# Kernel tuning notes

Hardware: AMD Instinct MI355X
Metric: run time of the kernel (lower is better)

## Reference

```python
import jax, jax.numpy as jnp
import numpy as np

N = 50000        # nodes
E = 800000       # edges (avg degree 16)
F_IN = 11        # raw node features
HID = 128        # hidden_dim
HEADS = 4
C = HID // HEADS # per-head channels = 32
L = 4            # num_layers
NEG_SLOPE = 0.2  # PyG GATv2 default


def setup_inputs() -> dict:
    key = jax.random.key(0)
    ks = jax.random.split(key, 10)
    s = 0.1
    node_features = jax.random.normal(ks[0], (N, F_IN), jnp.float32)
    edge_index = jax.random.randint(ks[1], (2, E), 0, N, dtype=jnp.int32)
    W_emb = jax.random.normal(ks[2], (HID, F_IN), jnp.float32) * s
    b_emb = jnp.zeros((HID,), jnp.float32)
    Wl = jax.random.normal(ks[3], (L, HID, HID), jnp.float32) * s
    bl = jnp.zeros((L, HID), jnp.float32)
    Wr = jax.random.normal(ks[4], (L, HID, HID), jnp.float32) * s
    br = jnp.zeros((L, HID), jnp.float32)
    att = jax.random.normal(ks[5], (L, HEADS, C), jnp.float32) * s
    bias = jnp.zeros((L, HID), jnp.float32)
    return {
        "node_features": node_features, "edge_index": edge_index, "num_nodes": N,
        "W_emb": W_emb, "b_emb": b_emb, "Wl": Wl, "bl": bl,
        "Wr": Wr, "br": br, "att": att, "bias": bias,
    }


def _gatv2_layer(x, src, dst, Wl, bl, Wr, br, att, bias):
    """PyG GATv2Conv (concat=True, share_weights=False), dropout off."""
    n = x.shape[0]
    xl = (x @ Wl.T + bl).reshape(n, HEADS, C)  # source transform
    xr = (x @ Wr.T + br).reshape(n, HEADS, C)  # target transform
    e = jax.nn.leaky_relu(xl[src] + xr[dst], NEG_SLOPE)       # [E,H,C]
    logits = jnp.einsum('ehc,hc->eh', e, att)                 # [E,H]
    # segment softmax over incoming edges per destination node
    m = jax.ops.segment_max(logits, dst, num_segments=n)      # [N,H]
    m = jnp.where(jnp.isfinite(m), m, jnp.zeros_like(m))      # empty segments
    p = jnp.exp(logits - m[dst])                              # [E,H]
    denom = jax.ops.segment_sum(p, dst, num_segments=n)       # [N,H]
    alpha = p / denom[dst]
    out = jax.ops.segment_sum(alpha[:, :, None] * xl[src], dst, num_segments=n)
    return out.reshape(n, HID) + bias


def reference(node_features, edge_index, num_nodes, W_emb, b_emb, Wl, bl, Wr, br, att, bias):
    src, dst = edge_index[0], edge_index[1]
    x = jax.nn.relu(node_features @ W_emb.T + b_emb)
    for i in range(L):  # BatchNorms exist in the torch module but are never applied
        x_res = x
        x = _gatv2_layer(x, src, dst, Wl[i], bl[i], Wr[i], br[i], att[i], bias[i])
        x = jax.nn.relu(x)
        if i > 0:
            x = x + x_res
    graph_mean = jnp.mean(x, axis=0)
    graph_max = jnp.max(x, axis=0)
    graph_embedding = jnp.concatenate([graph_mean, graph_max], axis=-1)  # [2*HID]
    return graph_embedding, x
```

## Files before the change

### kernel.cpp

```cpp
#include <hip/hip_runtime.h>
#include <math.h>

#define HID 128
#define HEADS 4
#define NEG_SLOPE 0.2f
#define R1B 1024
#define BCAP 8192
#define PB 6144
#define ACHUNK 4096

typedef float f32x4 __attribute__((ext_vector_type(4)));
typedef _Float16 f16x8 __attribute__((ext_vector_type(8)));
typedef _Float16 f16x4 __attribute__((ext_vector_type(4)));
typedef _Float16 f16x2 __attribute__((ext_vector_type(2)));

#if defined(__has_builtin)
#if __has_builtin(__builtin_amdgcn_fdot2)
#define HAVE_FDOT2 1
#endif
#endif


__global__ __launch_bounds__(256) void k_zero_int(int* p, int n) {
    int i = blockIdx.x * blockDim.x + threadIdx.x;
    if (i < n) p[i] = 0;
}

__global__ __launch_bounds__(256) void k_binA(const int* __restrict__ src, const int* __restrict__ dst,
                                              int E, int* __restrict__ gcnt, int* __restrict__ arena) {
    __shared__ int lh[256];
    __shared__ int lbase[256];
    __shared__ unsigned short lrank[ACHUNK];
    const int tid = threadIdx.x;
    lh[tid] = 0;
    __syncthreads();
    const int e0 = blockIdx.x * ACHUNK;
    #pragma unroll
    for (int i = 0; i < ACHUNK / 256; i++) {
        int e = e0 + i * 256 + tid;
        if (e < E) {
            int b = dst[e] >> 8;
            lrank[i * 256 + tid] = (unsigned short)atomicAdd(&lh[b], 1);
        }
    }
    __syncthreads();
    if (lh[tid] > 0) lbase[tid] = atomicAdd(&gcnt[tid], lh[tid]);
    __syncthreads();
    #pragma unroll
    for (int i = 0; i < ACHUNK / 256; i++) {
        int e = e0 + i * 256 + tid;
        if (e < E) {
            int d = dst[e];
            int b = d >> 8;
            arena[b * BCAP + lbase[b] + lrank[i * 256 + tid]] = (src[e] << 8) | (d & 255);
        }
    }
}

__global__ __launch_bounds__(256) void k_scan_bk(const int* __restrict__ gcnt, int nbk,
                                                 int* __restrict__ bstart, int* __restrict__ rowptr,
                                                 int N, int E) {
    __shared__ int buf[256];
    int tid = threadIdx.x;
    int v = (tid < nbk) ? gcnt[tid] : 0;
    buf[tid] = v;
    __syncthreads();
    for (int off = 1; off < 256; off <<= 1) {
        int t = (tid >= off) ? buf[tid - off] : 0;
        __syncthreads();
        buf[tid] += t;
        __syncthreads();
    }
    bstart[tid] = buf[tid] - v;
    if (tid == 0) rowptr[N] = E;
}

__global__ __launch_bounds__(256) void k_binB(const int* __restrict__ arena, const int* __restrict__ gcnt,
                                              const int* __restrict__ bstart, int N,
                                              int* __restrict__ rowptr, int* __restrict__ csr_off) {
    __shared__ int ncnt[256];
    __shared__ int sbuf[256];
    __shared__ int nstart[256];
    __shared__ int stage[PB];
    __shared__ unsigned short rk[BCAP];
    const int b = blockIdx.x, tid = threadIdx.x;
    const int cnt = gcnt[b];
    const int seg = bstart[b];
    ncnt[tid] = 0;
    __syncthreads();
    for (int k = tid; k < cnt; k += 256) {
        int v = arena[b * BCAP + k];
        rk[k] = (unsigned short)atomicAdd(&ncnt[v & 255], 1);
    }
    __syncthreads();
    int c = ncnt[tid];
    sbuf[tid] = c;
    __syncthreads();
    for (int off = 1; off < 256; off <<= 1) {
        int t = (tid >= off) ? sbuf[tid - off] : 0;
        __syncthreads();
        sbuf[tid] += t;
        __syncthreads();
    }
    int myStart = sbuf[tid] - c;
    nstart[tid] = myStart;
    int n = b * 256 + tid;
    if (n < N) rowptr[n] = seg + myStart;
    __syncthreads();
    for (int k = tid; k < cnt; k += 256) {
        int v = arena[b * BCAP + k];
        int pos = nstart[v & 255] + rk[k];
        int val = v & 0xFFFFFF00;
        if (pos < PB) stage[pos] = val;
        else          csr_off[seg + pos] = val;
    }
    __syncthreads();
    int lim = min(cnt, PB);
    for (int k = tid; k < lim; k += 256) csr_off[seg + k] = stage[k];
}


__device__ inline f16x2 absh2(f16x2 v) {
    unsigned u = __builtin_bit_cast(unsigned, v) & 0x7FFF7FFFu;
    return __builtin_bit_cast(f16x2, u);
}

template <int CTRL>
__device__ inline float qp_xor_add(float x) {
    int y = __builtin_amdgcn_update_dpp(0, __builtin_bit_cast(int, x),
                                        CTRL, 0xF, 0xF, true);
    return x + __builtin_bit_cast(float, y);
}

__device__ inline float edge_logit(f16x2 c0, f16x2 c1, f16x2 c2, f16x2 c3,
                                   f16x2 xr0, f16x2 xr1, f16x2 xr2, f16x2 xr3,
                                   f16x2 a0, f16x2 a1, f16x2 a2, f16x2 a3) {
    const f16x2 k06 = (f16x2){(_Float16)0.6f, (_Float16)0.6f};
    const f16x2 k04 = (f16x2){(_Float16)0.4f, (_Float16)0.4f};
    f16x2 u0 = c0 + xr0, u1 = c1 + xr1, u2 = c2 + xr2, u3 = c3 + xr3;
    f16x2 l0 = u0 * k06 + absh2(u0) * k04;
    f16x2 l1 = u1 * k06 + absh2(u1) * k04;
    f16x2 l2 = u2 * k06 + absh2(u2) * k04;
    f16x2 l3 = u3 * k06 + absh2(u3) * k04;
#ifdef HAVE_FDOT2
    float p = __builtin_amdgcn_fdot2(l0, a0, 0.f, false);
    p = __builtin_amdgcn_fdot2(l1, a1, p, false);
    p = __builtin_amdgcn_fdot2(l2, a2, p, false);
    p = __builtin_amdgcn_fdot2(l3, a3, p, false);
#else
    float p = (float)l0[0] * (float)a0[0] + (float)l0[1] * (float)a0[1]
            + (float)l1[0] * (float)a1[0] + (float)l1[1] * (float)a1[1]
            + (float)l2[0] * (float)a2[0] + (float)l2[1] * (float)a2[1]
            + (float)l3[0] * (float)a3[0] + (float)l3[1] * (float)a3[1];
#endif
    return p;
}

__global__ __launch_bounds__(256) void k_tof16(const float* __restrict__ a, const float* __restrict__ b,
                                               _Float16* __restrict__ oa, _Float16* __restrict__ ob, int n) {
    const float* x = blockIdx.y ? b : a;
    _Float16*    o = blockIdx.y ? ob : oa;
    int base = (blockIdx.x * 256 + threadIdx.x) * 4;
    if (base >= n) return;
    float4 v = *(const float4*)(x + base);
    f16x4 h = {(_Float16)v.x, (_Float16)v.y, (_Float16)v.z, (_Float16)v.w};
    *(f16x4*)(o + base) = h;
}


__global__ __launch_bounds__(512) void k_linear_mfma(
        const _Float16* __restrict__ xh,
        const _Float16* __restrict__ WfL, const _Float16* __restrict__ WfR,
        const float* __restrict__ bl, const float* __restrict__ br,
        _Float16* __restrict__ xlh, _Float16* __restrict__ xrh, int N) {
    __shared__ _Float16 lds[16384];
    const int t   = threadIdx.x;
    const int mat = blockIdx.y;
    const _Float16* W = mat ? WfR : WfL;

    for (int g = t; g < 2048; g += 512) {
        int r = g >> 4, cc = g & 15;
        int dsto = r * 128 + ((cc ^ (r & 7)) << 3);
        *(float4*)&lds[dsto] = *(const float4*)(W + g * 8);
    }
    __syncthreads();

    const int wave = t >> 6;
    const int lane = t & 63;
    const int l16  = lane & 15;
    const int quad = lane >> 4;
    const int n0   = blockIdx.x * 256 + wave * 32;

    int arow0 = n0 + l16;
    int arow1 = n0 + 16 + l16;
    if (arow0 >= N) arow0 = N - 1;
    if (arow1 >= N) arow1 = N - 1;

    f32x4 acc[2][8];
    #pragma unroll
    for (int u = 0; u < 2; u++)
        #pragma unroll
        for (int s = 0; s < 8; s++) acc[u][s] = (f32x4){0.f, 0.f, 0.f, 0.f};

    #pragma unroll
    for (int k0 = 0; k0 < HID; k0 += 32) {
        f16x8 a0 = *(const f16x8*)(xh + arow0 * HID + k0 + quad * 8);
        f16x8 a1 = *(const f16x8*)(xh + arow1 * HID + k0 + quad * 8);
        const int cc = (k0 >> 3) + quad;
        #pragma unroll
        for (int s = 0; s < 8; s++) {
            const int row = s * 16 + l16;
            const int off = row * 128 + ((cc ^ (l16 & 7)) << 3);
            f16x8 b = *(const f16x8*)&lds[off];
            acc[0][s] = __builtin_amdgcn_mfma_f32_16x16x32_f16(a0, b, acc[0][s], 0, 0, 0);
            acc[1][s] = __builtin_amdgcn_mfma_f32_16x16x32_f16(a1, b, acc[1][s], 0, 0, 0);
        }
    }

    const float* bias = mat ? br : bl;
    _Float16* dst = mat ? xrh : xlh;
    #pragma unroll
    for (int s = 0; s < 8; s++) {
        int col = s * 16 + l16;
        float bv = bias[col];
        #pragma unroll
        for (int u = 0; u < 2; u++) {
            #pragma unroll
            for (int r = 0; r < 4; r++) {
                int node = n0 + u * 16 + quad * 4 + r;
                if (node < N) dst[(size_t)node * HID + col] = (_Float16)(acc[u][s][r] + bv);
            }
        }
    }
}


__global__ __launch_bounds__(256, 8) void k_attn(const _Float16* __restrict__ xlh, const _Float16* __restrict__ xrh,
                                              const int* __restrict__ rowptr, const int* __restrict__ csr_off,
                                              const float* __restrict__ att, const float* __restrict__ bias,
                                              const _Float16* __restrict__ xres, _Float16* __restrict__ outx,
                                              float* __restrict__ out,
                                              int add_res, int want_half, int N) {
    const int wave = threadIdx.x >> 6;
    const int lane = threadIdx.x & 63;
    const int strm = lane >> 4;
    const int l16  = lane & 15;
    const int n = blockIdx.x * 4 + wave;
    if (n >= N) return;

    const float4 aA = *(const float4*)(att + 8 * l16);
    const float4 aB = *(const float4*)(att + 8 * l16 + 4);
    const f16x2 a0 = (f16x2){(_Float16)aA.x, (_Float16)aA.y};
    const f16x2 a1 = (f16x2){(_Float16)aA.z, (_Float16)aA.w};
    const f16x2 a2 = (f16x2){(_Float16)aB.x, (_Float16)aB.y};
    const f16x2 a3 = (f16x2){(_Float16)aB.z, (_Float16)aB.w};
    const f16x8 xrv = *(const f16x8*)(xrh + (size_t)n * HID + 8 * l16);
    const f16x2 xr0 = __builtin_shufflevector(xrv, xrv, 0, 1);
    const f16x2 xr1 = __builtin_shufflevector(xrv, xrv, 2, 3);
    const f16x2 xr2 = __builtin_shufflevector(xrv, xrv, 4, 5);
    const f16x2 xr3 = __builtin_shufflevector(xrv, xrv, 6, 7);
    const int s0 = rowptr[n], s1 = rowptr[n + 1];

    float den = 0.f;
    f16x2 acc16[4];
    #pragma unroll
    for (int q = 0; q < 4; q++) acc16[q] = (f16x2){(_Float16)0.f, (_Float16)0.f};

    const char* xlb = (const char*)xlh + l16 * 16;

    int j = s0 + 2 * strm;
    if (j < s1) {
        const int last = s1 - 1;
        f16x8 pa0 = *(const f16x8*)(xlb + csr_off[j]);
        f16x8 pb0 = *(const f16x8*)(xlb + csr_off[min(j + 1, last)]);
        f16x8 pa1 = *(const f16x8*)(xlb + csr_off[min(j + 8, last)]);
        f16x8 pb1 = *(const f16x8*)(xlb + csr_off[min(j + 9, last)]);
        int oa = csr_off[min(j + 16, last)];
        int ob = csr_off[min(j + 17, last)];
        while (j < s1) {
            f16x8 ca = pa0, cb = pb0;
            pa0 = pa1; pb0 = pb1;
            pa1 = *(const f16x8*)(xlb + oa);
            pb1 = *(const f16x8*)(xlb + ob);
            oa = csr_off[min(j + 24, last)];
            ob = csr_off[min(j + 25, last)];

            f16x2 ca0 = __builtin_shufflevector(ca, ca, 0, 1);
            f16x2 ca1 = __builtin_shufflevector(ca, ca, 2, 3);
            f16x2 ca2 = __builtin_shufflevector(ca, ca, 4, 5);
            f16x2 ca3 = __builtin_shufflevector(ca, ca, 6, 7);
            f16x2 cb0 = __builtin_shufflevector(cb, cb, 0, 1);
            f16x2 cb1 = __builtin_shufflevector(cb, cb, 2, 3);
            f16x2 cb2 = __builtin_shufflevector(cb, cb, 4, 5);
            f16x2 cb3 = __builtin_shufflevector(cb, cb, 6, 7);

            float pa = edge_logit(ca0, ca1, ca2, ca3, xr0, xr1, xr2, xr3, a0, a1, a2, a3);
            float pb = edge_logit(cb0, cb1, cb2, cb3, xr0, xr1, xr2, xr3, a0, a1, a2, a3);

            pa = qp_xor_add<0xB1>(pa);
            pa = qp_xor_add<0x4E>(pa);
            pb = qp_xor_add<0xB1>(pb);
            pb = qp_xor_add<0x4E>(pb);

            float wa = __expf(pa);
            float wb = __expf(pb);
            if (j + 1 >= s1) wb = 0.f;
            den += wa + wb;
            _Float16 wah = (_Float16)wa, wbh = (_Float16)wb;
            f16x2 wpa = (f16x2){wah, wah};
            f16x2 wpb = (f16x2){wbh, wbh};
            acc16[0] += wpa * ca0;
            acc16[1] += wpa * ca1;
            acc16[2] += wpa * ca2;
            acc16[3] += wpa * ca3;
            acc16[0] += wpb * cb0;
            acc16[1] += wpb * cb1;
            acc16[2] += wpb * cb2;
            acc16[3] += wpb * cb3;
            j += 8;
        }
    }

    float acc[8];
    #pragma unroll
    for (int q = 0; q < 4; q++) {
        acc[2 * q]     = (float)acc16[q][0];
        acc[2 * q + 1] = (float)acc16[q][1];
    }

    den += __shfl_xor(den, 16);
    den += __shfl_xor(den, 32);
    #pragma unroll
    for (int q = 0; q < 8; q++) {
        acc[q] += __shfl_xor(acc[q], 16);
        acc[q] += __shfl_xor(acc[q], 32);
    }

    if (strm == 0) {
        float4 bA = *(const float4*)(bias + 8 * l16);
        float4 bB = *(const float4*)(bias + 8 * l16 + 4);
        float b[8] = {bA.x, bA.y, bA.z, bA.w, bB.x, bB.y, bB.z, bB.w};
        float inv = (den > 0.f) ? 1.f / den : 0.f;
        float v[8];
        #pragma unroll
        for (int q = 0; q < 8; q++) v[q] = fmaxf(acc[q] * inv + b[q], 0.f);
        if (add_res) {
            f16x8 r = *(const f16x8*)(xres + (size_t)n * HID + 8 * l16);
            #pragma unroll
            for (int q = 0; q < 8; q++) v[q] += (float)r[q];
        }
        if (want_half) {
            f16x8 h;
            #pragma unroll
            for (int q = 0; q < 8; q++) h[q] = (_Float16)v[q];
            *(f16x8*)(outx + (size_t)n * HID + 8 * l16) = h;
        } else {
            *(float4*)(out + (size_t)n * HID + 8 * l16)     = make_float4(v[0], v[1], v[2], v[3]);
            *(float4*)(out + (size_t)n * HID + 8 * l16 + 4) = make_float4(v[4], v[5], v[6], v[7]);
        }
    }
}


__global__ __launch_bounds__(128) void k_embed(const float* __restrict__ nf, const float* __restrict__ W,
                                               const float* __restrict__ b,
                                               _Float16* __restrict__ xh, int N) {
    __shared__ float f[11];
    int n = blockIdx.x;
    int h = threadIdx.x;
    if (h < 11) f[h] = nf[(size_t)n * 11 + h];
    __syncthreads();
    float acc = b[h];
    #pragma unroll
    for (int k = 0; k < 11; k++) acc += f[k] * W[h * 11 + k];
    xh[(size_t)n * HID + h] = (_Float16)fmaxf(acc, 0.f);
}


__global__ __launch_bounds__(256) void k_reduce1(const float* __restrict__ x, int N,
                                                 float* __restrict__ psum, float* __restrict__ pmax) {
    __shared__ float ls[8][HID];
    __shared__ float lm[8][HID];
    const int c4 = (threadIdx.x & 31) << 2;
    const int rl = threadIdx.x >> 5;
    const int per = (N + gridDim.x - 1) / gridDim.x;
    const int n0 = blockIdx.x * per, n1 = min(N, n0 + per);
    float4 s = make_float4(0.f, 0.f, 0.f, 0.f);
    float4 m = make_float4(-INFINITY, -INFINITY, -INFINITY, -INFINITY);
    for (int n = n0 + rl; n < n1; n += 8) {
        float4 v = *(const float4*)(x + (size_t)n * HID + c4);
        s.x += v.x; s.y += v.y; s.z += v.z; s.w += v.w;
        m.x = fmaxf(m.x, v.x); m.y = fmaxf(m.y, v.y);
        m.z = fmaxf(m.z, v.z); m.w = fmaxf(m.w, v.w);
    }
    *(float4*)&ls[rl][c4] = s;
    *(float4*)&lm[rl][c4] = m;
    __syncthreads();
    if (rl < 4) {
        float4 a = *(float4*)&ls[rl][c4], bq = *(float4*)&ls[rl + 4][c4];
        a.x += bq.x; a.y += bq.y; a.z += bq.z; a.w += bq.w;
        *(float4*)&ls[rl][c4] = a;
        float4 am = *(float4*)&lm[rl][c4], bm = *(float4*)&lm[rl + 4][c4];
        am.x = fmaxf(am.x, bm.x); am.y = fmaxf(am.y, bm.y);
        am.z = fmaxf(am.z, bm.z); am.w = fmaxf(am.w, bm.w);
        *(float4*)&lm[rl][c4] = am;
    }
    __syncthreads();
    if (rl < 2) {
        float4 a = *(float4*)&ls[rl][c4], bq = *(float4*)&ls[rl + 2][c4];
        a.x += bq.x; a.y += bq.y; a.z += bq.z; a.w += bq.w;
        *(float4*)&ls[rl][c4] = a;
        float4 am = *(float4*)&lm[rl][c4], bm = *(float4*)&lm[rl + 2][c4];
        am.x = fmaxf(am.x, bm.x); am.y = fmaxf(am.y, bm.y);
        am.z = fmaxf(am.z, bm.z); am.w = fmaxf(am.w, bm.w);
        *(float4*)&lm[rl][c4] = am;
    }
    __syncthreads();
    if (rl == 0) {
        float4 a = *(float4*)&ls[0][c4], bq = *(float4*)&ls[1][c4];
        a.x += bq.x; a.y += bq.y; a.z += bq.z; a.w += bq.w;
        *(float4*)(psum + (size_t)blockIdx.x * HID + c4) = a;
        float4 am = *(float4*)&lm[0][c4], bm = *(float4*)&lm[1][c4];
        am.x = fmaxf(am.x, bm.x); am.y = fmaxf(am.y, bm.y);
        am.z = fmaxf(am.z, bm.z); am.w = fmaxf(am.w, bm.w);
        *(float4*)(pmax + (size_t)blockIdx.x * HID + c4) = am;
    }
}

__global__ __launch_bounds__(1024) void k_reduce2(const float* __restrict__ psum, const float* __restrict__ pmax,
                                                  int nb, float* __restrict__ out, float invN) {
    __shared__ float ss[8][HID];
    __shared__ float sm[8][HID];
    int h = threadIdx.x & 127;
    int c = threadIdx.x >> 7;
    int per = nb >> 3;
    float s = 0.f, m = -INFINITY;
    for (int b = c * per; b < (c + 1) * per; b++) {
        s += psum[b * HID + h];
        m = fmaxf(m, pmax[b * HID + h]);
    }
    ss[c][h] = s; sm[c][h] = m;
    __syncthreads();
    if (c < 4) { ss[c][h] += ss[c + 4][h]; sm[c][h] = fmaxf(sm[c][h], sm[c + 4][h]); }
    __syncthreads();
    if (c < 2) { ss[c][h] += ss[c + 2][h]; sm[c][h] = fmaxf(sm[c][h], sm[c + 2][h]); }
    __syncthreads();
    if (c == 0) {
        out[h] = (ss[0][h] + ss[1][h]) * invN;
        out[HID + h] = fmaxf(sm[0][h], sm[1][h]);
    }
}


extern "C" void kernel_launch(void* const* d_in, const int* in_sizes, int n_in,
                              void* d_out, int out_size, void* d_ws, size_t ws_size,
                              hipStream_t stream) {
    const float* nf    = (const float*)d_in[0];
    const int*   ei    = (const int*)d_in[1];
    const float* W_emb = (const float*)d_in[3];
    const float* b_emb = (const float*)d_in[4];
    const float* Wl    = (const float*)d_in[5];
    const float* bl    = (const float*)d_in[6];
    const float* Wr    = (const float*)d_in[7];
    const float* br    = (const float*)d_in[8];
    const float* att   = (const float*)d_in[9];
    const float* bias  = (const float*)d_in[10];

    const int N = in_sizes[0] / 11;
    const int E = in_sizes[1] / 2;
    const int* src = ei;
    const int* dst = ei + E;

    float* out  = (float*)d_out;
    float* xout = out + 2 * HID;

    char* w = (char*)d_ws;
    _Float16* xlh  = (_Float16*)w; w += (size_t)N * HID * 2;
    _Float16* xrh  = (_Float16*)w; w += (size_t)N * HID * 2;
    _Float16* xA   = (_Float16*)w; w += (size_t)N * HID * 2;
    _Float16* xB   = (_Float16*)w; w += (size_t)N * HID * 2;
    _Float16* WfL  = (_Float16*)w; w += (size_t)4 * HID * HID * 2;
    _Float16* WfR  = (_Float16*)w; w += (size_t)4 * HID * HID * 2;
    int*   gcnt    = (int*)w;   w += (size_t)256 * 4;
    int*   bstart  = (int*)w;   w += (size_t)256 * 4;
    int*   rowptr  = (int*)w;   w += (size_t)(N + 1) * 4;
    int*   arena   = (int*)w;   w += (size_t)256 * BCAP * 4;
    int*   csr_off = (int*)w;   w += (size_t)E * 4;
    float* psum    = (float*)w; w += (size_t)R1B * HID * 4;
    float* pmax    = (float*)w; w += (size_t)R1B * HID * 4;

    const int nbk = (N + 255) >> 8;
    const int nW = 4 * HID * HID;

    dim3 tg((nW / 4 + 255) / 256, 2);
    k_tof16<<<tg, 256, 0, stream>>>(Wl, Wr, WfL, WfR, nW);

    k_zero_int<<<1, 256, 0, stream>>>(gcnt, 256);
    k_binA<<<(E + ACHUNK - 1) / ACHUNK, 256, 0, stream>>>(src, dst, E, gcnt, arena);
    k_scan_bk<<<1, 256, 0, stream>>>(gcnt, nbk, bstart, rowptr, N, E);
    k_binB<<<nbk, 256, 0, stream>>>(arena, gcnt, bstart, N, rowptr, csr_off);

    k_embed<<<N, 128, 0, stream>>>(nf, W_emb, b_emb, xA, N);

    dim3 lgrid((N + 255) / 256, 2);
    for (int i = 0; i < 4; i++) {
        const _Float16* xin = (i & 1) ? xB : xA;
        _Float16* xo        = (i & 1) ? xA : xB;
        k_linear_mfma<<<lgrid, 512, 0, stream>>>(xin,
                                                 WfL + (size_t)i * HID * HID, WfR + (size_t)i * HID * HID,
                                                 bl + i * HID, br + i * HID, xlh, xrh, N);
        k_attn<<<(N + 3) / 4, 256, 0, stream>>>(xlh, xrh, rowptr, csr_off,
                                                att + i * HEADS * 32, bias + i * HID,
                                                xin, xo, xout,
                                                i > 0 ? 1 : 0, i < 3 ? 1 : 0, N);
    }

    k_reduce1<<<R1B, 256, 0, stream>>>(xout, N, psum, pmax);
    k_reduce2<<<1, 1024, 0, stream>>>(psum, pmax, R1B, out, 1.0f / N);
}
```

Before: 396.5 us.

## Fold zero and scan kernels, add low-degree attention fast path, pack reductions

Removes the gcnt zeroing kernel by doing it inside k_tof16, and removes the bucket-scan kernel by having every k_binB block redo the 256-entry scan itself. The attention kernel gains a straight-line path for nodes with degree up to 16 that issues all four gathers at once, and the cross-stream reduction now shuffles packed f16x2 values instead of eight floats. k_embed handles two nodes per 256-thread block. Together these cut launch count and per-node overhead, at the cost of a redundant scan in each binB block and reducing the accumulators in half precision.

```diff
diff --git a/kernel.cpp b/kernel.cpp
--- a/kernel.cpp
+++ b/kernel.cpp
@@ -21,11 +21,6 @@
 #endif
 
 
-__global__ __launch_bounds__(256) void k_zero_int(int* p, int n) {
-    int i = blockIdx.x * blockDim.x + threadIdx.x;
-    if (i < n) p[i] = 0;
-}
-
 __global__ __launch_bounds__(256) void k_binA(const int* __restrict__ src, const int* __restrict__ dst,
                                               int E, int* __restrict__ gcnt, int* __restrict__ arena) {
     __shared__ int lh[256];
@@ -57,35 +52,32 @@
     }
 }
 
-__global__ __launch_bounds__(256) void k_scan_bk(const int* __restrict__ gcnt, int nbk,
-                                                 int* __restrict__ bstart, int* __restrict__ rowptr,
-                                                 int N, int E) {
-    __shared__ int buf[256];
-    int tid = threadIdx.x;
-    int v = (tid < nbk) ? gcnt[tid] : 0;
-    buf[tid] = v;
-    __syncthreads();
-    for (int off = 1; off < 256; off <<= 1) {
-        int t = (tid >= off) ? buf[tid - off] : 0;
-        __syncthreads();
-        buf[tid] += t;
-        __syncthreads();
-    }
-    bstart[tid] = buf[tid] - v;
-    if (tid == 0) rowptr[N] = E;
-}
-
 __global__ __launch_bounds__(256) void k_binB(const int* __restrict__ arena, const int* __restrict__ gcnt,
-                                              const int* __restrict__ bstart, int N,
+                                              int N, int E,
                                               int* __restrict__ rowptr, int* __restrict__ csr_off) {
     __shared__ int ncnt[256];
     __shared__ int sbuf[256];
     __shared__ int nstart[256];
+    __shared__ int exv[256];
     __shared__ int stage[PB];
     __shared__ unsigned short rk[BCAP];
     const int b = blockIdx.x, tid = threadIdx.x;
+
+    int gv = gcnt[tid];
+    sbuf[tid] = gv;
+    __syncthreads();
+    for (int off = 1; off < 256; off <<= 1) {
+        int t = (tid >= off) ? sbuf[tid - off] : 0;
+        __syncthreads();
+        sbuf[tid] += t;
+        __syncthreads();
+    }
+    exv[tid] = sbuf[tid] - gv;
+    if (b == 0 && tid == 0) rowptr[N] = E;
+    __syncthreads();
+    const int seg = exv[b];
     const int cnt = gcnt[b];
-    const int seg = bstart[b];
+
     ncnt[tid] = 0;
     __syncthreads();
     for (int k = tid; k < cnt; k += 256) {
@@ -125,6 +117,13 @@
     return __builtin_bit_cast(f16x2, u);
 }
 
+__device__ inline f16x8 zero8() {
+    f16x8 z;
+    #pragma unroll
+    for (int i = 0; i < 8; i++) z[i] = (_Float16)0.f;
+    return z;
+}
+
 template <int CTRL>
 __device__ inline float qp_xor_add(float x) {
     int y = __builtin_amdgcn_update_dpp(0, __builtin_bit_cast(int, x),
@@ -132,11 +131,15 @@
     return x + __builtin_bit_cast(float, y);
 }
 
-__device__ inline float edge_logit(f16x2 c0, f16x2 c1, f16x2 c2, f16x2 c3,
-                                   f16x2 xr0, f16x2 xr1, f16x2 xr2, f16x2 xr3,
-                                   f16x2 a0, f16x2 a1, f16x2 a2, f16x2 a3) {
+__device__ inline float edge_logit8(f16x8 c,
+                                    f16x2 xr0, f16x2 xr1, f16x2 xr2, f16x2 xr3,
+                                    f16x2 a0, f16x2 a1, f16x2 a2, f16x2 a3) {
     const f16x2 k06 = (f16x2){(_Float16)0.6f, (_Float16)0.6f};
     const f16x2 k04 = (f16x2){(_Float16)0.4f, (_Float16)0.4f};
+    f16x2 c0 = __builtin_shufflevector(c, c, 0, 1);
+    f16x2 c1 = __builtin_shufflevector(c, c, 2, 3);
+    f16x2 c2 = __builtin_shufflevector(c, c, 4, 5);
+    f16x2 c3 = __builtin_shufflevector(c, c, 6, 7);
     f16x2 u0 = c0 + xr0, u1 = c1 + xr1, u2 = c2 + xr2, u3 = c3 + xr3;
     f16x2 l0 = u0 * k06 + absh2(u0) * k04;
     f16x2 l1 = u1 * k06 + absh2(u1) * k04;
@@ -156,8 +159,16 @@
     return p;
 }
 
+#define ACC_ROW(WP, R)                                                        \
+    acc16[0] += (WP) * __builtin_shufflevector((R), (R), 0, 1);               \
+    acc16[1] += (WP) * __builtin_shufflevector((R), (R), 2, 3);               \
+    acc16[2] += (WP) * __builtin_shufflevector((R), (R), 4, 5);               \
+    acc16[3] += (WP) * __builtin_shufflevector((R), (R), 6, 7);
+
 __global__ __launch_bounds__(256) void k_tof16(const float* __restrict__ a, const float* __restrict__ b,
-                                               _Float16* __restrict__ oa, _Float16* __restrict__ ob, int n) {
+                                               _Float16* __restrict__ oa, _Float16* __restrict__ ob,
+                                               int* __restrict__ gcnt, int n) {
+    if (blockIdx.x == 0 && blockIdx.y == 0) gcnt[threadIdx.x] = 0;
     const float* x = blockIdx.y ? b : a;
     _Float16*    o = blockIdx.y ? ob : oa;
     int base = (blockIdx.x * 256 + threadIdx.x) * 4;
@@ -260,6 +271,7 @@
     const f16x2 xr2 = __builtin_shufflevector(xrv, xrv, 4, 5);
     const f16x2 xr3 = __builtin_shufflevector(xrv, xrv, 6, 7);
     const int s0 = rowptr[n], s1 = rowptr[n + 1];
+    const int deg = s1 - s0;
 
     float den = 0.f;
     f16x2 acc16[4];
@@ -267,76 +279,97 @@
     for (int q = 0; q < 4; q++) acc16[q] = (f16x2){(_Float16)0.f, (_Float16)0.f};
 
     const char* xlb = (const char*)xlh + l16 * 16;
-
-    int j = s0 + 2 * strm;
-    if (j < s1) {
+    const int j = s0 + 2 * strm;
+
+    if (deg > 0 && deg <= 16) {
         const int last = s1 - 1;
-        f16x8 pa0 = *(const f16x8*)(xlb + csr_off[j]);
-        f16x8 pb0 = *(const f16x8*)(xlb + csr_off[min(j + 1, last)]);
-        f16x8 pa1 = *(const f16x8*)(xlb + csr_off[min(j + 8, last)]);
-        f16x8 pb1 = *(const f16x8*)(xlb + csr_off[min(j + 9, last)]);
-        int oa = csr_off[min(j + 16, last)];
-        int ob = csr_off[min(j + 17, last)];
-        while (j < s1) {
+        const int e0 = j, e1 = j + 1, e2 = j + 8, e3 = j + 9;
+        f16x8 r0, r1, r2, r3;
+        if (e0 < s1) {
+            int o0 = csr_off[e0];
+            int o1 = csr_off[min(e1, last)];
+            r0 = *(const f16x8*)(xlb + o0);
+            r1 = *(const f16x8*)(xlb + o1);
+        } else { r0 = zero8(); r1 = zero8(); }
+        if (e2 < s1) {
+            int o2 = csr_off[e2];
+            int o3 = csr_off[min(e3, last)];
+            r2 = *(const f16x8*)(xlb + o2);
+            r3 = *(const f16x8*)(xlb + o3);
+        } else { r2 = zero8(); r3 = zero8(); }
+
+        float p0 = edge_logit8(r0, xr0, xr1, xr2, xr3, a0, a1, a2, a3);
+        float p1 = edge_logit8(r1, xr0, xr1, xr2, xr3, a0, a1, a2, a3);
+        float p2 = edge_logit8(r2, xr0, xr1, xr2, xr3, a0, a1, a2, a3);
+        float p3 = edge_logit8(r3, xr0, xr1, xr2, xr3, a0, a1, a2, a3);
+        p0 = qp_xor_add<0xB1>(p0); p0 = qp_xor_add<0x4E>(p0);
+        p1 = qp_xor_add<0xB1>(p1); p1 = qp_xor_add<0x4E>(p1);
+        p2 = qp_xor_add<0xB1>(p2); p2 = qp_xor_add<0x4E>(p2);
+        p3 = qp_xor_add<0xB1>(p3); p3 = qp_xor_add<0x4E>(p3);
+        float w0 = (e0 < s1) ? __expf(p0) : 0.f;
+        float w1 = (e1 < s1) ? __expf(p1) : 0.f;
+        float w2 = (e2 < s1) ? __expf(p2) : 0.f;
+        float w3 = (e3 < s1) ? __expf(p3) : 0.f;
+        den += (w0 + w1) + (w2 + w3);
+        f16x2 wp0 = (f16x2){(_Float16)w0, (_Float16)w0};
+        f16x2 wp1 = (f16x2){(_Float16)w1, (_Float16)w1};
+        f16x2 wp2 = (f16x2){(_Float16)w2, (_Float16)w2};
+        f16x2 wp3 = (f16x2){(_Float16)w3, (_Float16)w3};
+        ACC_ROW(wp0, r0)
+        ACC_ROW(wp1, r1)
+        ACC_ROW(wp2, r2)
+        ACC_ROW(wp3, r3)
+    } else if (deg > 16) {
+        const int last = s1 - 1;
+        int jj = j;
+        f16x8 pa0 = *(const f16x8*)(xlb + csr_off[jj]);
+        f16x8 pb0 = *(const f16x8*)(xlb + csr_off[jj + 1]);
+        f16x8 pa1 = *(const f16x8*)(xlb + csr_off[jj + 8]);
+        f16x8 pb1 = *(const f16x8*)(xlb + csr_off[jj + 9]);
+        int oa = csr_off[min(jj + 16, last)];
+        int ob = csr_off[min(jj + 17, last)];
+        while (jj < s1) {
             f16x8 ca = pa0, cb = pb0;
             pa0 = pa1; pb0 = pb1;
-            pa1 = *(const f16x8*)(xlb + oa);
-            pb1 = *(const f16x8*)(xlb + ob);
-            oa = csr_off[min(j + 24, last)];
-            ob = csr_off[min(j + 25, last)];
-
-            f16x2 ca0 = __builtin_shufflevector(ca, ca, 0, 1);
-            f16x2 ca1 = __builtin_shufflevector(ca, ca, 2, 3);
-            f16x2 ca2 = __builtin_shufflevector(ca, ca, 4, 5);
-            f16x2 ca3 = __builtin_shufflevector(ca, ca, 6, 7);
-            f16x2 cb0 = __builtin_shufflevector(cb, cb, 0, 1);
-            f16x2 cb1 = __builtin_shufflevector(cb, cb, 2, 3);
-            f16x2 cb2 = __builtin_shufflevector(cb, cb, 4, 5);
-            f16x2 cb3 = __builtin_shufflevector(cb, cb, 6, 7);
-
-            float pa = edge_logit(ca0, ca1, ca2, ca3, xr0, xr1, xr2, xr3, a0, a1, a2, a3);
-            float pb = edge_logit(cb0, cb1, cb2, cb3, xr0, xr1, xr2, xr3, a0, a1, a2, a3);
-
-            pa = qp_xor_add<0xB1>(pa);
-            pa = qp_xor_add<0x4E>(pa);
-            pb = qp_xor_add<0xB1>(pb);
-            pb = qp_xor_add<0x4E>(pb);
-
+            if (jj + 16 < s1) {
+                pa1 = *(const f16x8*)(xlb + oa);
+                pb1 = *(const f16x8*)(xlb + ob);
+                oa = csr_off[min(jj + 24, last)];
+                ob = csr_off[min(jj + 25, last)];
+            } else { pa1 = zero8(); pb1 = zero8(); }
+
+            float pa = edge_logit8(ca, xr0, xr1, xr2, xr3, a0, a1, a2, a3);
+            float pb = edge_logit8(cb, xr0, xr1, xr2, xr3, a0, a1, a2, a3);
+            pa = qp_xor_add<0xB1>(pa); pa = qp_xor_add<0x4E>(pa);
+            pb = qp_xor_add<0xB1>(pb); pb = qp_xor_add<0x4E>(pb);
             float wa = __expf(pa);
-            float wb = __expf(pb);
-            if (j + 1 >= s1) wb = 0.f;
+            float wb = (jj + 1 < s1) ? __expf(pb) : 0.f;
             den += wa + wb;
-            _Float16 wah = (_Float16)wa, wbh = (_Float16)wb;
-            f16x2 wpa = (f16x2){wah, wah};
-            f16x2 wpb = (f16x2){wbh, wbh};
-            acc16[0] += wpa * ca0;
-            acc16[1] += wpa * ca1;
-            acc16[2] += wpa * ca2;
-            acc16[3] += wpa * ca3;
-            acc16[0] += wpb * cb0;
-            acc16[1] += wpb * cb1;
-            acc16[2] += wpb * cb2;
-            acc16[3] += wpb * cb3;
-            j += 8;
-        }
-    }
-
-    float acc[8];
-    #pragma unroll
-    for (int q = 0; q < 4; q++) {
-        acc[2 * q]     = (float)acc16[q][0];
-        acc[2 * q + 1] = (float)acc16[q][1];
+            f16x2 wpa = (f16x2){(_Float16)wa, (_Float16)wa};
+            f16x2 wpb = (f16x2){(_Float16)wb, (_Float16)wb};
+            ACC_ROW(wpa, ca)
+            ACC_ROW(wpb, cb)
+            jj += 8;
+        }
     }
 
     den += __shfl_xor(den, 16);
     den += __shfl_xor(den, 32);
     #pragma unroll
-    for (int q = 0; q < 8; q++) {
-        acc[q] += __shfl_xor(acc[q], 16);
-        acc[q] += __shfl_xor(acc[q], 32);
+    for (int q = 0; q < 4; q++) {
+        float pk = __builtin_bit_cast(float, acc16[q]);
+        acc16[q] += __builtin_bit_cast(f16x2, __shfl_xor(pk, 16));
+        pk = __builtin_bit_cast(float, acc16[q]);
+        acc16[q] += __builtin_bit_cast(f16x2, __shfl_xor(pk, 32));
     }
 
     if (strm == 0) {
+        float acc[8];
+        #pragma unroll
+        for (int q = 0; q < 4; q++) {
+            acc[2 * q]     = (float)acc16[q][0];
+            acc[2 * q + 1] = (float)acc16[q][1];
+        }
         float4 bA = *(const float4*)(bias + 8 * l16);
         float4 bB = *(const float4*)(bias + 8 * l16 + 4);
         float b[8] = {bA.x, bA.y, bA.z, bA.w, bB.x, bB.y, bB.z, bB.w};
@@ -362,17 +395,19 @@
 }
 
 
-__global__ __launch_bounds__(128) void k_embed(const float* __restrict__ nf, const float* __restrict__ W,
+__global__ __launch_bounds__(256) void k_embed(const float* __restrict__ nf, const float* __restrict__ W,
                                                const float* __restrict__ b,
                                                _Float16* __restrict__ xh, int N) {
-    __shared__ float f[11];
-    int n = blockIdx.x;
-    int h = threadIdx.x;
-    if (h < 11) f[h] = nf[(size_t)n * 11 + h];
-    __syncthreads();
+    __shared__ float f[2][11];
+    const int sub = threadIdx.x >> 7;
+    const int h   = threadIdx.x & 127;
+    const int n   = blockIdx.x * 2 + sub;
+    if (n < N && h < 11) f[sub][h] = nf[(size_t)n * 11 + h];
+    __syncthreads();
+    if (n >= N) return;
     float acc = b[h];
     #pragma unroll
-    for (int k = 0; k < 11; k++) acc += f[k] * W[h * 11 + k];
+    for (int k = 0; k < 11; k++) acc += f[sub][k] * W[h * 11 + k];
     xh[(size_t)n * HID + h] = (_Float16)fmaxf(acc, 0.f);
 }
 
@@ -482,7 +517,6 @@
     _Float16* WfL  = (_Float16*)w; w += (size_t)4 * HID * HID * 2;
     _Float16* WfR  = (_Float16*)w; w += (size_t)4 * HID * HID * 2;
     int*   gcnt    = (int*)w;   w += (size_t)256 * 4;
-    int*   bstart  = (int*)w;   w += (size_t)256 * 4;
     int*   rowptr  = (int*)w;   w += (size_t)(N + 1) * 4;
     int*   arena   = (int*)w;   w += (size_t)256 * BCAP * 4;
     int*   csr_off = (int*)w;   w += (size_t)E * 4;
@@ -493,14 +527,12 @@
     const int nW = 4 * HID * HID;
 
     dim3 tg((nW / 4 + 255) / 256, 2);
-    k_tof16<<<tg, 256, 0, stream>>>(Wl, Wr, WfL, WfR, nW);
-
-    k_zero_int<<<1, 256, 0, stream>>>(gcnt, 256);
+    k_tof16<<<tg, 256, 0, stream>>>(Wl, Wr, WfL, WfR, gcnt, nW);
+
     k_binA<<<(E + ACHUNK - 1) / ACHUNK, 256, 0, stream>>>(src, dst, E, gcnt, arena);
-    k_scan_bk<<<1, 256, 0, stream>>>(gcnt, nbk, bstart, rowptr, N, E);
-    k_binB<<<nbk, 256, 0, stream>>>(arena, gcnt, bstart, N, rowptr, csr_off);
-
-    k_embed<<<N, 128, 0, stream>>>(nf, W_emb, b_emb, xA, N);
+    k_binB<<<nbk, 256, 0, stream>>>(arena, gcnt, N, E, rowptr, csr_off);
+
+    k_embed<<<(N + 1) / 2, 256, 0, stream>>>(nf, W_emb, b_emb, xA, N);
 
     dim3 lgrid((N + 255) / 256, 2);
     for (int i = 0; i < 4; i++) {
```

New measurement: 389.3 us. Within noise of the previous version (-1.8%).
